# Kernel optimization log

Measured on AMD Instinct MI355X. Metric: run time of the kernel, lower is better.

Reference implementation:

```python
import jax, jax.numpy as jnp
import numpy as np

EPS = 1e-5
BIG = np.int32(2 ** 30)      # sentinel larger than any voxel label
L_MAX = 1024                  # fixed upper bound on number of components (jit-friendly)


def _offsets(conn):
    # 3D neighborhood offsets with at most `conn` nonzero coordinates (skimage connectivity)
    offs = []
    for dz in (-1, 0, 1):
        for dy in (-1, 0, 1):
            for dx in (-1, 0, 1):
                nz = (dz != 0) + (dy != 0) + (dx != 0)
                if 0 < nz <= conn:
                    offs.append((dz, dy, dx))
    return offs


def _ccl_26(fg):
    """Connected-component labeling, 26-connectivity (skimage.label connectivity=3).
    Iterative min-label propagation (3x3x3 min-pool) + pointer jumping.
    Returns int32 labels: 0 = background, each component gets min(flat_index)+1."""
    shape = fg.shape
    n = fg.size
    init = jnp.where(fg, jnp.arange(1, n + 1, dtype=jnp.int32).reshape(shape), 0)

    def step(labels):
        cand = jnp.where(fg, labels, BIG)
        pooled = jax.lax.reduce_window(cand, BIG, jax.lax.min, (3, 3, 3), (1, 1, 1), 'SAME')
        new = jnp.where(fg, jnp.minimum(labels, pooled), 0)
        flat = new.ravel()
        for _ in range(2):  # pointer jumping / path compression (labels are flat_index+1)
            parent = flat[jnp.maximum(flat - 1, 0)]
            flat = jnp.where(flat > 0, parent, 0)
        return flat.reshape(shape)

    def cond(c):
        old, new = c
        return jnp.any(old != new)

    def body(c):
        _, cur = c
        return cur, step(cur)

    _, final = jax.lax.while_loop(cond, body, (init, step(init)))
    return final


def _inner_boundary_18(fg):
    """skimage find_boundaries(mode='inner', connectivity=2) on 3D binary mask:
    foreground voxel with any background voxel in its 18-neighborhood
    (fg & ~erosion(fg), reflect border handling)."""
    D, H, W = fg.shape
    p = jnp.pad(fg, 1, mode='reflect')
    eroded = fg
    for dz, dy, dx in _offsets(2):
        eroded = eroded & p[1 + dz:1 + dz + D, 1 + dy:1 + dy + H, 1 + dx:1 + dx + W]
    return fg & ~eroded


def _compactness(y_pred):
    fg = y_pred > 0.5
    labels = _ccl_26(fg)                       # [D,H,W] int32
    boundary = _inner_boundary_18(fg)          # [D,H,W] bool

    # compact per-component ids (sorted unique labels, padded with BIG to stay sorted)
    uniq = jnp.unique(labels, size=L_MAX, fill_value=BIG)
    ids = jnp.searchsorted(uniq, labels).astype(jnp.int32)

    area = jax.ops.segment_sum(fg.astype(jnp.float32).ravel(), ids.ravel(), num_segments=L_MAX)
    perim = jax.ops.segment_sum(boundary.astype(jnp.float32).ravel(), ids.ravel(), num_segments=L_MAX)

    valid = (uniq > 0) & (uniq < BIG)
    # sum over z of 4*pi*area_z / (perim_3d^2 + eps) == 4*pi*total_area / (perim^2 + eps),
    # then averaged over depth D (as in the original per-label /= shape[0]).
    per_label = jnp.where(valid, 4.0 * jnp.pi * area / (perim ** 2 + EPS), 0.0)
    return jnp.sum(per_label) / y_pred.shape[0]


def setup_inputs() -> dict:
    key = jax.random.key(0)
    y_pred = jax.random.uniform(key, (64, 256, 256), dtype=jnp.float32)
    return {"y_pred": y_pred}


def reference(y_pred) -> jnp.ndarray:
    comp = _compactness(y_pred)
    return 1.0 / (comp + EPS)
```

## Files before the change

### kernel.cpp

```cpp
#include <hip/hip_runtime.h>

#define DD 64
#define HH 256
#define WW 256
#define NN (DD*HH*WW)
#define GHS 4096
#define PHS 131072
#define NSEG (NN/32)

#define TZ 8
#define TY 32
#define TX 32
#define TVOX (TZ*TY*TX)

#define CA 458752
#define CB 114688
#define CFACE (CA + 4*CB)

__device__ const signed char Foff[27][3] = {
  {-1,-1,-1},{-1,-1,0},{-1,-1,1},{-1,0,-1},{-1,0,0},{-1,0,1},{-1,1,-1},{-1,1,0},{-1,1,1},
  {-1,-1,-1},{-1,-1,0},{-1,-1,1},{0,-1,-1},{0,-1,0},{0,-1,1},
  {-1,1,-1},{-1,1,0},{-1,1,1},
  {-1,-1,-1},{-1,0,-1},{-1,1,-1},{0,-1,-1},{0,0,-1},
  {-1,-1,1},{-1,0,1},{-1,1,1},{0,-1,1}};
__device__ const int Fst[5] = {0, 9, 15, 18, 23};
__device__ const int Fct[5] = {9, 6, 3, 5, 4};

__device__ __forceinline__ int ufind(int* P, int x){
  int p = P[x];
  while (p != x){
    int gp = P[p];
    if (gp != p) P[x] = gp;
    x = gp;
    p = P[x];
  }
  return x;
}

__device__ __forceinline__ int ufind_ro(const int* P, int x){
  int p = P[x];
  while (p != x){ x = p; p = P[x]; }
  return x;
}

__device__ __forceinline__ void uunion(int* P, int a, int b){
  while (true){
    a = ufind(P, a);
    b = ufind(P, b);
    if (a == b) return;
    if (a < b){ int t = a; a = b; b = t; }
    int old = atomicMin(&P[a], b);
    if (old == a) return;
    a = old;
  }
}

__device__ __forceinline__ int run_start(unsigned m, int x){
  unsigned zb = (~m) & ((x == 0) ? 0u : ((1u << x) - 1u));
  return (zb == 0) ? 0 : (32 - __builtin_clz(zb));
}

__device__ __forceinline__ int refl(int v, int L){ return v < 0 ? 1 : (v >= L ? L - 2 : v); }

__global__ __launch_bounds__(1024) void k_local(const float* __restrict__ in,
                                                int* __restrict__ parent,
                                                unsigned* __restrict__ fgbits,
                                                int* __restrict__ hkey,
                                                int* __restrict__ harea,
                                                int* __restrict__ hper,
                                                unsigned long long* __restrict__ ph){
  __shared__ int sl[TVOX];
  __shared__ unsigned srow[256];
  const int t = threadIdx.x;
  const int b = blockIdx.x;
  const int z0 = (b >> 6) * TZ;
  const int y0 = ((b >> 3) & 7) * TY;
  const int x0 = (b & 7) * TX;

  if (b < GHS / 1024){ int j = b * 1024 + t; hkey[j] = -1; harea[j] = 0; hper[j] = 0; }
  { int j = b * 1024 + t; if (j < PHS) ph[j] = ~0ULL; }

  const int row = t >> 2;
  const int xb  = (t & 3) * 8;
  const int lz  = row >> 5, ly = row & 31;
  const int gi0 = ((z0 + lz) << 16) | ((y0 + ly) << 8) | (x0 + xb);

  float4 f0 = *(const float4*)(in + gi0);
  float4 f1 = *(const float4*)(in + gi0 + 4);
  int by = (f0.x > 0.5f)        | ((f0.y > 0.5f) << 1) |
           ((f0.z > 0.5f) << 2) | ((f0.w > 0.5f) << 3) |
           ((f1.x > 0.5f) << 4) | ((f1.y > 0.5f) << 5) |
           ((f1.z > 0.5f) << 6) | ((f1.w > 0.5f) << 7);
  int v1 = by | (__shfl_xor(by, 1) << 8);
  int v2 = v1 | (__shfl_xor(v1, 2) << 16);
  if ((t & 3) == 0){
    srow[row] = (unsigned)v2;
    fgbits[((z0 + lz) << 11) | ((y0 + ly) << 3) | (x0 >> 5)] = (unsigned)v2;
  }
  __syncthreads();

  const unsigned m = srow[row];
  const unsigned starts = m & ~(m << 1);
  const unsigned sm = starts & (0xFFu << xb);

  {
    unsigned w = sm;
    while (w){
      int s = __builtin_ctz(w); w &= w - 1;
      sl[(row << 5) | s] = (row << 5) | s;
    }
  }
  __syncthreads();

  const int rel[4][2] = {{-1,-1},{-1,0},{-1,1},{0,-1}};
  {
    unsigned w0 = sm;
    while (w0){
      int x = __builtin_ctz(w0); w0 &= w0 - 1;
      unsigned zs = (~m) >> x;
      int len = zs ? __builtin_ctz(zs) : (32 - x);
      int end = x + len - 1;
      unsigned long long wmask = ((1ull << (end + 2)) - 1) &
                                 ~((x == 0) ? 0ull : ((1ull << (x - 1)) - 1));
      int self = (row << 5) | x;
      #pragma unroll
      for (int r = 0; r < 4; r++){
        int zz = lz + rel[r][0], yy = ly + rel[r][1];
        if (zz < 0 || yy < 0 || yy >= TY) continue;
        int nrow = (zz << 5) | yy;
        unsigned mN = srow[nrow];
        unsigned wm = mN & (unsigned)wmask;
        while (wm){
          int bb = __builtin_ctz(wm);
          int ns = run_start(mN, bb);
          uunion(sl, self, (nrow << 5) | ns);
          unsigned t2 = (~mN) >> bb;
          int l2 = t2 ? __builtin_ctz(t2) : (32 - bb);
          unsigned long long clr = (bb + l2 >= 32) ? 0xffffffffull : ((1ull << (bb + l2)) - 1);
          wm &= ~(unsigned)clr;
        }
      }
    }
  }
  __syncthreads();

  {
    unsigned w = sm;
    while (w){
      int s = __builtin_ctz(w); w &= w - 1;
      int v = (row << 5) | s;
      sl[v] = ufind_ro(sl, v);
    }
  }
  __syncthreads();

  int lab[8];
  int cur = -1;
  #pragma unroll
  for (int k = 0; k < 8; k++){
    int x = xb + k;
    if (!((m >> x) & 1)){ lab[k] = -1; cur = -1; continue; }
    if (cur < 0){
      int rs = (k == 0) ? run_start(m, x) : x;
      int r = sl[(row << 5) | rs];
      cur = ((z0 + (r >> 10)) << 16) | ((y0 + ((r >> 5) & 31)) << 8) | (x0 + (r & 31));
    }
    lab[k] = cur;
  }
  *(int4*)(parent + gi0)     = make_int4(lab[0], lab[1], lab[2], lab[3]);
  *(int4*)(parent + gi0 + 4) = make_int4(lab[4], lab[5], lab[6], lab[7]);
}

__device__ __forceinline__ void phash_union(unsigned long long* H, unsigned long long key,
                                            int* parent){
  unsigned h = (unsigned)((key * 0x9E3779B97F4A7C15ull) >> 47);
  while (true){
    unsigned long long old = atomicCAS(&H[h], ~0ULL, key);
    if (old == ~0ULL){ uunion(parent, (int)(key >> 32), (int)(key & 0xffffffffu)); return; }
    if (old == key) return;
    h = (h + 1) & (PHS - 1);
  }
}

__global__ __launch_bounds__(256) void k_pairs(int* __restrict__ parent,
                                               const unsigned* __restrict__ fgbits,
                                               unsigned long long* __restrict__ ph){
  __shared__ unsigned long long pk[256];
  const int t = threadIdx.x;
  pk[t] = ~0ULL;
  __syncthreads();

  const int id = blockIdx.x * 256 + t;
  int z, y, x, ot;
  if (id < CA){ ot = 0; z = ((id >> 16) + 1) << 3; y = (id >> 8) & 255; x = id & 255; }
  else {
    int q = id - CA;
    int f = q >> 14;
    int r = q & 16383;
    int g = f / 7, mm = f % 7;
    if      (g == 0){ ot = 1; y = (mm + 1) << 5;  z = r >> 8; x = r & 255; }
    else if (g == 1){ ot = 2; y = (mm << 5) + 31; z = r >> 8; x = r & 255; }
    else if (g == 2){ ot = 3; x = (mm + 1) << 5;  z = r >> 8; y = r & 255; }
    else            { ot = 4; x = (mm << 5) + 31; z = r >> 8; y = r & 255; }
  }
  const int i = (z << 16) | (y << 8) | x;
  if ((fgbits[(z << 11) | (y << 3) | (x >> 5)] >> (x & 31)) & 1){
    int a = parent[i];
    const int st = Fst[ot], en = st + Fct[ot];
    for (int k = st; k < en; k++){
      int zz = z + Foff[k][0], yy = y + Foff[k][1], xx = x + Foff[k][2];
      if (zz < 0 || yy < 0 || yy >= HH || xx < 0 || xx >= WW) continue;
      if (!((fgbits[(zz << 11) | (yy << 3) | (xx >> 5)] >> (xx & 31)) & 1)) continue;
      int bl = parent[(zz << 16) | (yy << 8) | xx];
      int hi = a > bl ? a : bl, lo = a > bl ? bl : a;
      unsigned long long key = ((unsigned long long)(unsigned)hi << 32) | (unsigned)lo;
      unsigned h = (unsigned)((key * 0x9E3779B97F4A7C15ull) >> 56);
      bool done = false;
      for (int probe = 0; probe < 256; probe++){
        unsigned long long old = atomicCAS(&pk[h], ~0ULL, key);
        if (old == ~0ULL || old == key){ done = true; break; }
        h = (h + 1) & 255;
      }
      if (!done) phash_union(ph, key, parent);
    }
  }
  __syncthreads();
  if (pk[t] != ~0ULL) phash_union(ph, pk[t], parent);
}

__device__ __forceinline__ void ghash_add(int* hkey, int* harea, int* hper,
                                          int key, int a, int p){
  unsigned h = ((unsigned)key * 2654435761u) >> 20;
  while (true){
    int old = atomicCAS(&hkey[h], -1, key);
    if (old == -1 || old == key){
      atomicAdd(&harea[h], a);
      if (p) atomicAdd(&hper[h], p);
      return;
    }
    h = (h + 1) & (GHS - 1);
  }
}

__global__ __launch_bounds__(1024) void k_stats(int* __restrict__ parent,
                                                const unsigned* __restrict__ fgbits,
                                                int* __restrict__ hkey,
                                                int* __restrict__ harea,
                                                int* __restrict__ hper){
  __shared__ unsigned sfg[144];
  __shared__ unsigned sbnd[32];
  __shared__ int sk[256], sa[256], sp[256];
  const int t = threadIdx.x;
  const int b = blockIdx.x;
  const int z = b >> 6;
  const int y0 = (b & 63) * 4;

  if (t < 256){ sk[t] = -1; sa[t] = 0; sp[t] = 0; }
  if (t < 144){
    int p = t / 48, q = (t / 8) % 6, s = t & 7;
    int zz = refl(z + p - 1, DD), yy = refl(y0 + q - 1, HH);
    sfg[t] = fgbits[(zz << 11) | (yy << 3) | s];
  }
  __syncthreads();

  if (t < 32){
    int ry = t >> 3, s = t & 7;
    auto W  = [&](int p, int q){ return sfg[p * 48 + q * 8 + s]; };
    auto WL = [&](int p, int q){
      unsigned w = W(p, q);
      unsigned c = (s > 0) ? ((sfg[p * 48 + q * 8 + s - 1] >> 31) & 1u) : ((w >> 1) & 1u);
      return (w << 1) | c;
    };
    auto WR = [&](int p, int q){
      unsigned w = W(p, q);
      unsigned c = (s < 7) ? ((sfg[p * 48 + q * 8 + s + 1] & 1u) << 31) : ((w & 0x40000000u) << 1);
      return (w >> 1) | c;
    };
    int qm = ry, qc = ry + 1, qp = ry + 2;
    unsigned own = W(1, qc);
    unsigned e = W(0, qm) & W(0, qp) & W(2, qm) & W(2, qp);
    e &= W(0, qc) & WL(0, qc) & WR(0, qc);
    e &= W(2, qc) & WL(2, qc) & WR(2, qc);
    e &= W(1, qm) & WL(1, qm) & WR(1, qm);
    e &= W(1, qp) & WL(1, qp) & WR(1, qp);
    e &= WL(1, qc) & WR(1, qc);
    sbnd[t] = own & ~e;
  }
  __syncthreads();

  const int i = b * 1024 + t;
  int lab = parent[i];
  int bnd = 0;
  if (lab >= 0) bnd = (sbnd[t >> 5] >> (t & 31)) & 1;

  const int lane = t & 63;
  unsigned long long fgm = __ballot(lab >= 0);
  unsigned long long bm  = __ballot(bnd != 0);
  unsigned long long act = fgm;
  while (act){
    int leader = (int)__ffsll(act) - 1;
    int llab = __shfl(lab, leader);
    unsigned long long match = __ballot(lab == llab) & fgm;
    if (lane == leader){
      int r = ufind(parent, llab);
      int a = (int)__popcll(match);
      int p = (int)__popcll(match & bm);
      unsigned h = ((unsigned)r * 2654435761u) >> 24;
      bool done = false;
      for (int probe = 0; probe < 256; probe++){
        int old = atomicCAS(&sk[h], -1, r);
        if (old == -1 || old == r){
          atomicAdd(&sa[h], a);
          if (p) atomicAdd(&sp[h], p);
          done = true; break;
        }
        h = (h + 1) & 255;
      }
      if (!done) ghash_add(hkey, harea, hper, r, a, p);
    }
    act &= ~match;
  }
  __syncthreads();
  if (t < 256 && sk[t] >= 0) ghash_add(hkey, harea, hper, sk[t], sa[t], sp[t]);
}

__global__ void k_final(const int* __restrict__ hkey, const int* __restrict__ harea,
                        const int* __restrict__ hper, float* __restrict__ out){
  __shared__ float ssum[256];
  int t = threadIdx.x;
  float s = 0.0f;
  for (int j = t; j < GHS; j += 256){
    if (hkey[j] >= 0){
      float a = (float)harea[j];
      float p = (float)hper[j];
      s += 12.566370614359172f * a / (p * p + 1e-5f);
    }
  }
  ssum[t] = s;
  __syncthreads();
  for (int w = 128; w > 0; w >>= 1){
    if (t < w) ssum[t] += ssum[t + w];
    __syncthreads();
  }
  if (t == 0){
    float comp = ssum[0] / 64.0f;
    out[0] = 1.0f / (comp + 1e-5f);
  }
}

extern "C" void kernel_launch(void* const* d_in, const int* in_sizes, int n_in,
                              void* d_out, int out_size, void* d_ws, size_t ws_size,
                              hipStream_t stream){
  const float* y = (const float*)d_in[0];
  char* w = (char*)d_ws;
  int* parent            = (int*)w;                    w += (size_t)NN * 4;
  unsigned long long* ph = (unsigned long long*)w;     w += (size_t)PHS * 8;
  int* hkey              = (int*)w;                    w += GHS * 4;
  int* harea             = (int*)w;                    w += GHS * 4;
  int* hper              = (int*)w;                    w += GHS * 4;
  unsigned* fgbits       = (unsigned*)w;               w += (size_t)NSEG * 4;
  float* out = (float*)d_out;

  hipLaunchKernelGGL(k_local, dim3(512),       dim3(1024), 0, stream, y, parent, fgbits, hkey, harea, hper, ph);
  hipLaunchKernelGGL(k_pairs, dim3(CFACE/256), dim3(256),  0, stream, parent, fgbits, ph);
  hipLaunchKernelGGL(k_stats, dim3(NN/1024),   dim3(1024), 0, stream, parent, fgbits, hkey, harea, hper);
  hipLaunchKernelGGL(k_final, dim3(1),         dim3(256),  0, stream, hkey, harea, hper, out);
}
```

Measured before the change: 186.0 us.

## Privatize global stats hash into 16 copies and resolve roots per thread

```diff
diff --git a/kernel.cpp b/kernel.cpp
--- a/kernel.cpp
+++ b/kernel.cpp
@@ -5,6 +5,7 @@
 #define WW 256
 #define NN (DD*HH*WW)
 #define GHS 4096
+#define NCOPY 16
 #define PHS 131072
 #define NSEG (NN/32)
 
@@ -77,7 +78,7 @@
   const int y0 = ((b >> 3) & 7) * TY;
   const int x0 = (b & 7) * TX;
 
-  if (b < GHS / 1024){ int j = b * 1024 + t; hkey[j] = -1; harea[j] = 0; hper[j] = 0; }
+  if (b < (NCOPY * GHS) / 1024){ int j = b * 1024 + t; hkey[j] = -1; harea[j] = 0; hper[j] = 0; }
   { int j = b * 1024 + t; if (j < PHS) ph[j] = ~0ULL; }
 
   const int row = t >> 2;
@@ -242,7 +243,7 @@
   }
 }
 
-__global__ __launch_bounds__(1024) void k_stats(int* __restrict__ parent,
+__global__ __launch_bounds__(1024) void k_stats(const int* __restrict__ parent,
                                                 const unsigned* __restrict__ fgbits,
                                                 int* __restrict__ hkey,
                                                 int* __restrict__ harea,
@@ -291,7 +292,11 @@
   const int i = b * 1024 + t;
   int lab = parent[i];
   int bnd = 0;
-  if (lab >= 0) bnd = (sbnd[t >> 5] >> (t & 31)) & 1;
+  if (lab >= 0){
+    bnd = (sbnd[t >> 5] >> (t & 31)) & 1;
+    int p = parent[lab];
+    while (p != lab){ lab = p; p = parent[lab]; }
+  }
 
   const int lane = t & 63;
   unsigned long long fgm = __ballot(lab >= 0);
@@ -302,37 +307,58 @@
     int llab = __shfl(lab, leader);
     unsigned long long match = __ballot(lab == llab) & fgm;
     if (lane == leader){
-      int r = ufind(parent, llab);
       int a = (int)__popcll(match);
       int p = (int)__popcll(match & bm);
-      unsigned h = ((unsigned)r * 2654435761u) >> 24;
+      unsigned h = ((unsigned)llab * 2654435761u) >> 24;
       bool done = false;
       for (int probe = 0; probe < 256; probe++){
-        int old = atomicCAS(&sk[h], -1, r);
-        if (old == -1 || old == r){
+        int old = atomicCAS(&sk[h], -1, llab);
+        if (old == -1 || old == llab){
           atomicAdd(&sa[h], a);
           if (p) atomicAdd(&sp[h], p);
           done = true; break;
         }
         h = (h + 1) & 255;
       }
-      if (!done) ghash_add(hkey, harea, hper, r, a, p);
+      if (!done) ghash_add(hkey, harea, hper, llab, a, p);
     }
     act &= ~match;
   }
   __syncthreads();
-  if (t < 256 && sk[t] >= 0) ghash_add(hkey, harea, hper, sk[t], sa[t], sp[t]);
-}
-
-__global__ void k_final(const int* __restrict__ hkey, const int* __restrict__ harea,
-                        const int* __restrict__ hper, float* __restrict__ out){
+  const int c = (b & (NCOPY - 1)) * GHS;
+  if (t < 256 && sk[t] >= 0) ghash_add(hkey + c, harea + c, hper + c, sk[t], sa[t], sp[t]);
+}
+
+__global__ __launch_bounds__(256) void k_final(const int* __restrict__ hkey,
+                                               const int* __restrict__ harea,
+                                               const int* __restrict__ hper,
+                                               float* __restrict__ out){
+  __shared__ int mk[GHS], ma[GHS], mp[GHS];
   __shared__ float ssum[256];
-  int t = threadIdx.x;
+  const int t = threadIdx.x;
+  for (int j = t; j < GHS; j += 256){ mk[j] = -1; ma[j] = 0; mp[j] = 0; }
+  __syncthreads();
+  for (int j = t; j < NCOPY * GHS; j += 256){
+    int key = hkey[j];
+    if (key >= 0){
+      unsigned h = ((unsigned)key * 2654435761u) >> 20;
+      while (true){
+        int old = atomicCAS(&mk[h], -1, key);
+        if (old == -1 || old == key){
+          atomicAdd(&ma[h], harea[j]);
+          atomicAdd(&mp[h], hper[j]);
+          break;
+        }
+        h = (h + 1) & (GHS - 1);
+      }
+    }
+  }
+  __syncthreads();
   float s = 0.0f;
   for (int j = t; j < GHS; j += 256){
-    if (hkey[j] >= 0){
-      float a = (float)harea[j];
-      float p = (float)hper[j];
+    if (mk[j] >= 0){
+      float a = (float)ma[j];
+      float p = (float)mp[j];
       s += 12.566370614359172f * a / (p * p + 1e-5f);
     }
   }
@@ -355,9 +381,9 @@
   char* w = (char*)d_ws;
   int* parent            = (int*)w;                    w += (size_t)NN * 4;
   unsigned long long* ph = (unsigned long long*)w;     w += (size_t)PHS * 8;
-  int* hkey              = (int*)w;                    w += GHS * 4;
-  int* harea             = (int*)w;                    w += GHS * 4;
-  int* hper              = (int*)w;                    w += GHS * 4;
+  int* hkey              = (int*)w;                    w += (size_t)NCOPY * GHS * 4;
+  int* harea             = (int*)w;                    w += (size_t)NCOPY * GHS * 4;
+  int* hper              = (int*)w;                    w += (size_t)NCOPY * GHS * 4;
   unsigned* fgbits       = (unsigned*)w;               w += (size_t)NSEG * 4;
   float* out = (float*)d_out;
 
```

New measurement: 238.0 us. 1.28x slower.
